# Kernel optimization log

Measured on AMD Instinct MI355X. Metric: run time of the kernel, lower is better.

## Reference

```python
import jax, jax.numpy as jnp
import numpy as np

N_NODES = 100000
N_EDGES = 1600000
IN_FEATS = 256
OUT_FEATS = 64


def setup_inputs() -> dict:
    key = jax.random.key(0)
    k1, k2, k3, k4, k5, k6 = jax.random.split(key, 6)
    x = jax.random.normal(k1, (N_NODES, IN_FEATS), dtype=jnp.float32)
    edge_src = jax.random.randint(k2, (N_EDGES,), 0, N_NODES, dtype=jnp.int32)
    edge_dst = jax.random.randint(k3, (N_EDGES,), 0, N_NODES, dtype=jnp.int32)
    edge_weight = jax.random.uniform(k4, (N_EDGES,), dtype=jnp.float32)
    # Linear(in_feats, out_feats) params (Kaiming-uniform-ish init scale)
    scale = 1.0 / np.sqrt(IN_FEATS)
    W = jax.random.uniform(k5, (IN_FEATS, OUT_FEATS), minval=-scale, maxval=scale, dtype=jnp.float32)
    b = jax.random.uniform(k6, (OUT_FEATS,), minval=-scale, maxval=scale, dtype=jnp.float32)
    return {"x": x, "edge_src": edge_src, "edge_dst": edge_dst,
            "edge_weight": edge_weight, "W": W, "b": b}


def reference(x, edge_src, edge_dst, edge_weight, W, b):
    # h = fc(x)
    h = x @ W + b                                   # [N, out_feats]
    # spmm(graph, h): out[dst] += w * h[src]  (weighted adjacency matvec)
    msgs = h[edge_src] * edge_weight[:, None]       # [E, out_feats]
    out = jax.ops.segment_sum(msgs, edge_dst, num_segments=N_NODES)
    return out
```

## Files before the change

### kernel.cpp

```cpp
#include <hip/hip_runtime.h>

#define IN_F 256
#define OUT_F 64
#define SORT_CHUNK 4096
#define BKT_SHIFT 7
#define BKT_NODES 128
#define MAX_NB 1024

typedef __attribute__((ext_vector_type(8))) short short8;
typedef __attribute__((ext_vector_type(4))) float f32x4;

static __device__ __forceinline__ short f2bf(float f) {
    union { float f; unsigned u; } v; v.f = f;
    unsigned r = v.u + 0x7FFFu + ((v.u >> 16) & 1u);
    return (short)(r >> 16);
}
static __device__ __forceinline__ float bf2f(short s) {
    return __int_as_float(((unsigned)(unsigned short)s) << 16);
}

__global__ __launch_bounds__(256)
void prep_w_kernel(const float* __restrict__ W, short* __restrict__ Wt) {
    int i = blockIdx.x * 256 + threadIdx.x;
    if (i < IN_F * OUT_F) {
        int k = i / OUT_F, n = i % OUT_F;
        Wt[n * IN_F + k] = f2bf(W[i]);
    }
}

__global__ __launch_bounds__(256, 4)
void fc_mfma_kernel(const float* __restrict__ x, const short* __restrict__ Wt,
                    const float* __restrict__ b, short* __restrict__ h, int nRows) {
    __shared__ short Wl[OUT_F * IN_F];
    {
        const uint4* src = (const uint4*)Wt;
        #pragma unroll
        for (int it = 0; it < 8; ++it) {
            int g = it * 256 + threadIdx.x;
            int n = g >> 5, s = g & 31;
            *(uint4*)((char*)Wl + n * 512 + (s ^ (n & 7)) * 16) = src[g];
        }
    }
    __syncthreads();

    const int wv = threadIdx.x >> 6;
    const int l  = threadIdx.x & 63;
    const int lr = l & 15;
    const int kg = l >> 4;

    const int rowbase = (blockIdx.x * 4 + wv) * 32;
    if (rowbase >= nRows) return;

    const int ar0 = min(rowbase + lr,      nRows - 1);
    const int ar1 = min(rowbase + 16 + lr, nRows - 1);
    const float* xp0 = x + (size_t)ar0 * IN_F + kg * 8;
    const float* xp1 = x + (size_t)ar1 * IN_F + kg * 8;

    f32x4 acc[2][4];
    #pragma unroll
    for (int m = 0; m < 2; ++m)
        #pragma unroll
        for (int n = 0; n < 4; ++n) acc[m][n] = (f32x4)0.f;

    #pragma unroll
    for (int kt = 0; kt < 8; ++kt) {
        const int K0 = kt * 32;
        float4 a0lo = *(const float4*)(xp0 + K0);
        float4 a0hi = *(const float4*)(xp0 + K0 + 4);
        float4 a1lo = *(const float4*)(xp1 + K0);
        float4 a1hi = *(const float4*)(xp1 + K0 + 4);

        short8 a0, a1;
        a0[0] = f2bf(a0lo.x); a0[1] = f2bf(a0lo.y);
        a0[2] = f2bf(a0lo.z); a0[3] = f2bf(a0lo.w);
        a0[4] = f2bf(a0hi.x); a0[5] = f2bf(a0hi.y);
        a0[6] = f2bf(a0hi.z); a0[7] = f2bf(a0hi.w);
        a1[0] = f2bf(a1lo.x); a1[1] = f2bf(a1lo.y);
        a1[2] = f2bf(a1lo.z); a1[3] = f2bf(a1lo.w);
        a1[4] = f2bf(a1hi.x); a1[5] = f2bf(a1hi.y);
        a1[6] = f2bf(a1hi.z); a1[7] = f2bf(a1hi.w);

        short8 bf[4];
        #pragma unroll
        for (int nt = 0; nt < 4; ++nt) {
            const int col = nt * 16 + lr;
            const int slot = (kt * 4 + kg) ^ (col & 7);
            bf[nt] = *(const short8*)((const char*)Wl + col * 512 + slot * 16);
        }
        #pragma unroll
        for (int nt = 0; nt < 4; ++nt) {
            acc[0][nt] = __builtin_amdgcn_mfma_f32_16x16x32_bf16(a0, bf[nt], acc[0][nt], 0, 0, 0);
            acc[1][nt] = __builtin_amdgcn_mfma_f32_16x16x32_bf16(a1, bf[nt], acc[1][nt], 0, 0, 0);
        }
    }

    #pragma unroll
    for (int m = 0; m < 2; ++m) {
        #pragma unroll
        for (int nt = 0; nt < 4; ++nt) {
            const int col = nt * 16 + lr;
            const float bias = b[col];
            #pragma unroll
            for (int j = 0; j < 4; ++j) {
                const int r = rowbase + m * 16 + kg * 4 + j;
                if (r < nRows)
                    h[(size_t)r * OUT_F + col] = f2bf(acc[m][nt][j] + bias);
            }
        }
    }
}

__global__ __launch_bounds__(256)
void bhist_kernel(const int* __restrict__ dst, int* __restrict__ counts,
                  int nE, int NB, int nSB) {
    __shared__ int lh[MAX_NB];
    for (int b = threadIdx.x; b < NB; b += 256) lh[b] = 0;
    __syncthreads();
    int base = blockIdx.x * SORT_CHUNK;
    int lim = min(nE, base + SORT_CHUNK);
    for (int e = base + threadIdx.x; e < lim; e += 256)
        atomicAdd(&lh[dst[e] >> BKT_SHIFT], 1);
    __syncthreads();
    for (int b = threadIdx.x; b < NB; b += 256)
        counts[b * nSB + blockIdx.x] = lh[b];
}

__global__ __launch_bounds__(256)
void scan1_kernel(const int* __restrict__ cnt, int* __restrict__ off,
                  int* __restrict__ part, int n) {
    __shared__ int sh[256];
    int base = blockIdx.x * 1024;
    int t = threadIdx.x;
    int v[4]; int s = 0;
    #pragma unroll
    for (int i = 0; i < 4; ++i) {
        int idx = base + t * 4 + i;
        v[i] = (idx < n) ? cnt[idx] : 0;
        s += v[i];
    }
    sh[t] = s;
    __syncthreads();
    for (int d = 1; d < 256; d <<= 1) {
        int val = (t >= d) ? sh[t - d] : 0;
        __syncthreads();
        sh[t] += val;
        __syncthreads();
    }
    if (t == 255) part[blockIdx.x] = sh[255];
    int run = (t == 0) ? 0 : sh[t - 1];
    #pragma unroll
    for (int i = 0; i < 4; ++i) {
        int idx = base + t * 4 + i;
        if (idx < n) off[idx] = run;
        run += v[i];
    }
}

__global__ __launch_bounds__(256)
void scan2_kernel(int* __restrict__ part, int nPart) {
    __shared__ int sh[256];
    int t = threadIdx.x;
    int v[4]; int s = 0;
    #pragma unroll
    for (int i = 0; i < 4; ++i) {
        int idx = t * 4 + i;
        v[i] = (idx < nPart) ? part[idx] : 0;
        s += v[i];
    }
    sh[t] = s;
    __syncthreads();
    for (int d = 1; d < 256; d <<= 1) {
        int val = (t >= d) ? sh[t - d] : 0;
        __syncthreads();
        sh[t] += val;
        __syncthreads();
    }
    int run = (t == 0) ? 0 : sh[t - 1];
    #pragma unroll
    for (int i = 0; i < 4; ++i) {
        int idx = t * 4 + i;
        if (idx < nPart) part[idx] = run;
        run += v[i];
    }
}

__global__ __launch_bounds__(256)
void scan3_kernel(int* __restrict__ off, const int* __restrict__ part, int n) {
    for (int i = blockIdx.x * blockDim.x + threadIdx.x; i < n;
         i += gridDim.x * blockDim.x)
        off[i] += part[i >> 10];
}

__global__ __launch_bounds__(256)
void bfill_kernel(const int* __restrict__ src, const int* __restrict__ dst,
                  const float* __restrict__ w, const int* __restrict__ bases,
                  int2* __restrict__ pack, int nE, int NB, int nSB) {
    __shared__ int cur[MAX_NB];
    for (int b = threadIdx.x; b < NB; b += 256)
        cur[b] = bases[b * nSB + blockIdx.x];
    __syncthreads();
    int base = blockIdx.x * SORT_CHUNK;
    int lim = min(nE, base + SORT_CHUNK);
    for (int e = base + threadIdx.x; e < lim; e += 256) {
        int d = dst[e];
        int p = atomicAdd(&cur[d >> BKT_SHIFT], 1);
        pack[p] = make_int2(src[e] | ((d & (BKT_NODES - 1)) << 17),
                            __float_as_int(w[e]));
    }
}

__global__ __launch_bounds__(256)
void nsort_kernel(const int2* __restrict__ pack, const int* __restrict__ bases,
                  int2* __restrict__ pack2, int* __restrict__ off,
                  int nRows, int nE, int NB, int nSB) {
    __shared__ int cnt[BKT_NODES];
    __shared__ int scn[BKT_NODES];
    const int b = blockIdx.x;
    const int tid = threadIdx.x;
    const int segStart = bases[b * nSB];
    const int segEnd = (b + 1 < NB) ? bases[(b + 1) * nSB] : nE;

    if (tid < BKT_NODES) cnt[tid] = 0;
    __syncthreads();
    for (int e = segStart + tid; e < segEnd; e += 256)
        atomicAdd(&cnt[(pack[e].x >> 17) & (BKT_NODES - 1)], 1);
    __syncthreads();

    if (tid < BKT_NODES) scn[tid] = cnt[tid];
    __syncthreads();
    for (int d = 1; d < BKT_NODES; d <<= 1) {
        int t = 0;
        if (tid < BKT_NODES && tid >= d) t = scn[tid - d];
        __syncthreads();
        if (tid < BKT_NODES) scn[tid] += t;
        __syncthreads();
    }

    const int node0 = b * BKT_NODES;
    const int ncnt = min(BKT_NODES, nRows - node0);
    if (tid < ncnt)
        off[node0 + tid] = segStart + scn[tid] - cnt[tid];
    if (tid == 0 && node0 + ncnt == nRows)
        off[nRows] = segEnd;
    __syncthreads();

    if (tid < BKT_NODES) cnt[tid] = segStart + scn[tid] - cnt[tid];
    __syncthreads();
    for (int e = segStart + tid; e < segEnd; e += 256) {
        int2 p = pack[e];
        int dl = (p.x >> 17) & (BKT_NODES - 1);
        int q = atomicAdd(&cnt[dl], 1);
        pack2[q] = make_int2(p.x & 0x1FFFF, p.y);
    }
}

__global__ __launch_bounds__(256)
void ngather_kernel(const short* __restrict__ h, const int* __restrict__ off,
                    const int2* __restrict__ pack2, float* __restrict__ out,
                    int nNodes) {
    int wid = (blockIdx.x * 256 + threadIdx.x) >> 6;
    int lane = threadIdx.x & 63;
    if (wid >= nNodes) return;
    int e = off[wid], end = off[wid + 1];
    const ushort* hu = (const ushort*)h;
    float acc = 0.f;
    for (; e + 8 <= end; e += 8) {
        int2 pk[8];
        #pragma unroll
        for (int i = 0; i < 8; ++i) pk[i] = pack2[e + i];
        float hv[8];
        #pragma unroll
        for (int i = 0; i < 8; ++i)
            hv[i] = bf2f((short)hu[(size_t)pk[i].x * OUT_F + lane]);
        #pragma unroll
        for (int i = 0; i < 8; ++i)
            acc = fmaf(__int_as_float(pk[i].y), hv[i], acc);
    }
    for (; e + 4 <= end; e += 4) {
        int2 pk[4];
        #pragma unroll
        for (int i = 0; i < 4; ++i) pk[i] = pack2[e + i];
        #pragma unroll
        for (int i = 0; i < 4; ++i)
            acc = fmaf(__int_as_float(pk[i].y),
                       bf2f((short)hu[(size_t)pk[i].x * OUT_F + lane]), acc);
    }
    for (; e < end; ++e) {
        int2 p = pack2[e];
        acc = fmaf(__int_as_float(p.y),
                   bf2f((short)hu[(size_t)p.x * OUT_F + lane]), acc);
    }
    out[(size_t)wid * OUT_F + lane] = acc;
}

__global__ __launch_bounds__(256)
void scatter_kernel(const short* __restrict__ h, const int* __restrict__ src,
                    const int* __restrict__ dst, const float* __restrict__ w,
                    float* __restrict__ out, int nE) {
    int t = blockIdx.x * 256 + threadIdx.x;
    int c = t & 15;
    int stride = (gridDim.x * 256) >> 4;
    for (int e = t >> 4; e < nE; e += stride) {
        int s = src[e];
        int d = dst[e];
        float ww = w[e];
        float* op = out + (size_t)d * OUT_F + c * 4;
        const short* hp = h + (size_t)s * OUT_F + c * 4;
        unsafeAtomicAdd(op + 0, ww * bf2f(hp[0]));
        unsafeAtomicAdd(op + 1, ww * bf2f(hp[1]));
        unsafeAtomicAdd(op + 2, ww * bf2f(hp[2]));
        unsafeAtomicAdd(op + 3, ww * bf2f(hp[3]));
    }
}

static inline size_t align256(size_t x) { return (x + 255) & ~(size_t)255; }

extern "C" void kernel_launch(void* const* d_in, const int* in_sizes, int n_in,
                              void* d_out, int out_size, void* d_ws, size_t ws_size,
                              hipStream_t stream) {
    const float* x    = (const float*)d_in[0];
    const int*   esrc = (const int*)d_in[1];
    const int*   edst = (const int*)d_in[2];
    const float* ew   = (const float*)d_in[3];
    const float* W    = (const float*)d_in[4];
    const float* b    = (const float*)d_in[5];

    int nRows = in_sizes[0] / IN_F;
    int nE    = in_sizes[1];

    int NB  = (nRows + BKT_NODES - 1) / BKT_NODES;
    int nSB = (nE + SORT_CHUNK - 1) / SORT_CHUNK;
    int nCnt = NB * nSB;
    int nPart = (nCnt + 1023) / 1024;

    char* p = (char*)d_ws;
    size_t hB    = align256((size_t)nRows * OUT_F * sizeof(short));
    size_t wtB   = align256((size_t)IN_F * OUT_F * sizeof(short));
    size_t cntB  = align256((size_t)nCnt * sizeof(int));
    size_t basB  = align256((size_t)nCnt * sizeof(int));
    size_t partB = align256((size_t)nPart * sizeof(int));
    size_t packB = align256((size_t)nE * sizeof(int2));
    size_t offB  = align256((size_t)(nRows + 1) * sizeof(int));
    size_t need  = hB + wtB + cntB + basB + partB + 2 * packB + offB;

    short* h      = (short*)p;  p += hB;
    short* Wt     = (short*)p;  p += wtB;
    int*   counts = (int*)p;    p += cntB;
    int*   bases  = (int*)p;    p += basB;
    int*   part   = (int*)p;    p += partB;
    int2*  pack   = (int2*)p;   p += packB;
    int2*  pack2  = (int2*)p;   p += packB;
    int*   off    = (int*)p;

    float* out = (float*)d_out;

    prep_w_kernel<<<(IN_F * OUT_F + 255) / 256, 256, 0, stream>>>(W, Wt);
    int fcBlocks = (nRows + 127) / 128;
    fc_mfma_kernel<<<fcBlocks, 256, 0, stream>>>(x, Wt, b, h, nRows);

    bool ok = (ws_size >= need) && (NB <= MAX_NB) && (nPart <= 1024) &&
              (nRows < (1 << 17));
    if (ok) {
        bhist_kernel<<<nSB, 256, 0, stream>>>(edst, counts, nE, NB, nSB);
        scan1_kernel<<<nPart, 256, 0, stream>>>(counts, bases, part, nCnt);
        scan2_kernel<<<1, 256, 0, stream>>>(part, nPart);
        scan3_kernel<<<512, 256, 0, stream>>>(bases, part, nCnt);
        bfill_kernel<<<nSB, 256, 0, stream>>>(esrc, edst, ew, bases, pack,
                                              nE, NB, nSB);
        nsort_kernel<<<NB, 256, 0, stream>>>(pack, bases, pack2, off,
                                             nRows, nE, NB, nSB);
        int gBlocks = (nRows * 64 + 255) / 256;
        ngather_kernel<<<gBlocks, 256, 0, stream>>>(h, off, pack2, out, nRows);
    } else {
        hipMemsetAsync(out, 0, (size_t)out_size * sizeof(float), stream);
        scatter_kernel<<<4096, 256, 0, stream>>>(h, esrc, edst, ew, out, nE);
    }
}
```

Measured before the change: 307.2 us.

## Fuse histogram into FC kernel, fold scan3 into consumers, vectorize sort loops

The bucket histogram now runs as extra blocks of the FC MFMA kernel, so the two independent stages overlap in one launch. The scan3 pass is removed: bfill and nsort add the partial block offset themselves when reading bases. The histogram, bfill and nsort loops are vectorized or unrolled by four to put more loads in flight. This removes two launches and one pass over the offset array, at the cost of more complex kernels. Mixing the two block types in one grid may also change how the FC blocks are scheduled.

```diff
diff --git a/kernel.cpp b/kernel.cpp
--- a/kernel.cpp
+++ b/kernel.cpp
@@ -29,9 +29,35 @@
 }
 
 __global__ __launch_bounds__(256, 4)
-void fc_mfma_kernel(const float* __restrict__ x, const short* __restrict__ Wt,
-                    const float* __restrict__ b, short* __restrict__ h, int nRows) {
-    __shared__ short Wl[OUT_F * IN_F];
+void fc_bhist_kernel(const float* __restrict__ x, const short* __restrict__ Wt,
+                     const float* __restrict__ bias, short* __restrict__ h,
+                     const int* __restrict__ dst, int* __restrict__ counts,
+                     int nRows, int nE, int NB, int nSB, int nHist) {
+    __shared__ __align__(16) char smem[OUT_F * IN_F * sizeof(short)];
+    if ((int)blockIdx.x < nHist) {
+        int* lh = (int*)smem;
+        const int cb = blockIdx.x;
+        for (int b0 = threadIdx.x; b0 < NB; b0 += 256) lh[b0] = 0;
+        __syncthreads();
+        const int base = cb * SORT_CHUNK;
+        const int lim = min(nE, base + SORT_CHUNK);
+        const int4* d4 = (const int4*)(dst + base);
+        const int n4 = (lim - base) >> 2;
+        for (int i = threadIdx.x; i < n4; i += 256) {
+            int4 v = d4[i];
+            atomicAdd(&lh[v.x >> BKT_SHIFT], 1);
+            atomicAdd(&lh[v.y >> BKT_SHIFT], 1);
+            atomicAdd(&lh[v.z >> BKT_SHIFT], 1);
+            atomicAdd(&lh[v.w >> BKT_SHIFT], 1);
+        }
+        for (int e = base + (n4 << 2) + threadIdx.x; e < lim; e += 256)
+            atomicAdd(&lh[dst[e] >> BKT_SHIFT], 1);
+        __syncthreads();
+        for (int b0 = threadIdx.x; b0 < NB; b0 += 256)
+            counts[b0 * nSB + cb] = lh[b0];
+        return;
+    }
+    short* Wl = (short*)smem;
     {
         const uint4* src = (const uint4*)Wt;
         #pragma unroll
@@ -48,7 +74,8 @@
     const int lr = l & 15;
     const int kg = l >> 4;
 
-    const int rowbase = (blockIdx.x * 4 + wv) * 32;
+    const int fb = blockIdx.x - nHist;
+    const int rowbase = (fb * 4 + wv) * 32;
     if (rowbase >= nRows) return;
 
     const int ar0 = min(rowbase + lr,      nRows - 1);
@@ -99,30 +126,15 @@
         #pragma unroll
         for (int nt = 0; nt < 4; ++nt) {
             const int col = nt * 16 + lr;
-            const float bias = b[col];
+            const float bb = bias[col];
             #pragma unroll
             for (int j = 0; j < 4; ++j) {
                 const int r = rowbase + m * 16 + kg * 4 + j;
                 if (r < nRows)
-                    h[(size_t)r * OUT_F + col] = f2bf(acc[m][nt][j] + bias);
+                    h[(size_t)r * OUT_F + col] = f2bf(acc[m][nt][j] + bb);
             }
         }
     }
-}
-
-__global__ __launch_bounds__(256)
-void bhist_kernel(const int* __restrict__ dst, int* __restrict__ counts,
-                  int nE, int NB, int nSB) {
-    __shared__ int lh[MAX_NB];
-    for (int b = threadIdx.x; b < NB; b += 256) lh[b] = 0;
-    __syncthreads();
-    int base = blockIdx.x * SORT_CHUNK;
-    int lim = min(nE, base + SORT_CHUNK);
-    for (int e = base + threadIdx.x; e < lim; e += 256)
-        atomicAdd(&lh[dst[e] >> BKT_SHIFT], 1);
-    __syncthreads();
-    for (int b = threadIdx.x; b < NB; b += 256)
-        counts[b * nSB + blockIdx.x] = lh[b];
 }
 
 __global__ __launch_bounds__(256)
@@ -185,23 +197,35 @@
 }
 
 __global__ __launch_bounds__(256)
-void scan3_kernel(int* __restrict__ off, const int* __restrict__ part, int n) {
-    for (int i = blockIdx.x * blockDim.x + threadIdx.x; i < n;
-         i += gridDim.x * blockDim.x)
-        off[i] += part[i >> 10];
-}
-
-__global__ __launch_bounds__(256)
 void bfill_kernel(const int* __restrict__ src, const int* __restrict__ dst,
                   const float* __restrict__ w, const int* __restrict__ bases,
-                  int2* __restrict__ pack, int nE, int NB, int nSB) {
+                  const int* __restrict__ part, int2* __restrict__ pack,
+                  int nE, int NB, int nSB) {
     __shared__ int cur[MAX_NB];
-    for (int b = threadIdx.x; b < NB; b += 256)
-        cur[b] = bases[b * nSB + blockIdx.x];
-    __syncthreads();
-    int base = blockIdx.x * SORT_CHUNK;
-    int lim = min(nE, base + SORT_CHUNK);
-    for (int e = base + threadIdx.x; e < lim; e += 256) {
+    const int cb = blockIdx.x;
+    for (int b0 = threadIdx.x; b0 < NB; b0 += 256) {
+        int idx = b0 * nSB + cb;
+        cur[b0] = bases[idx] + part[idx >> 10];
+    }
+    __syncthreads();
+    const int base = cb * SORT_CHUNK;
+    const int lim = min(nE, base + SORT_CHUNK);
+    const int4* s4 = (const int4*)(src + base);
+    const int4* d4 = (const int4*)(dst + base);
+    const float4* w4 = (const float4*)(w + base);
+    const int n4 = (lim - base) >> 2;
+    for (int i = threadIdx.x; i < n4; i += 256) {
+        int4 s = s4[i]; int4 d = d4[i]; float4 ww = w4[i];
+        int p0 = atomicAdd(&cur[d.x >> BKT_SHIFT], 1);
+        pack[p0] = make_int2(s.x | ((d.x & (BKT_NODES - 1)) << 17), __float_as_int(ww.x));
+        int p1 = atomicAdd(&cur[d.y >> BKT_SHIFT], 1);
+        pack[p1] = make_int2(s.y | ((d.y & (BKT_NODES - 1)) << 17), __float_as_int(ww.y));
+        int p2 = atomicAdd(&cur[d.z >> BKT_SHIFT], 1);
+        pack[p2] = make_int2(s.z | ((d.z & (BKT_NODES - 1)) << 17), __float_as_int(ww.z));
+        int p3 = atomicAdd(&cur[d.w >> BKT_SHIFT], 1);
+        pack[p3] = make_int2(s.w | ((d.w & (BKT_NODES - 1)) << 17), __float_as_int(ww.w));
+    }
+    for (int e = base + (n4 << 2) + threadIdx.x; e < lim; e += 256) {
         int d = dst[e];
         int p = atomicAdd(&cur[d >> BKT_SHIFT], 1);
         pack[p] = make_int2(src[e] | ((d & (BKT_NODES - 1)) << 17),
@@ -211,19 +235,35 @@
 
 __global__ __launch_bounds__(256)
 void nsort_kernel(const int2* __restrict__ pack, const int* __restrict__ bases,
-                  int2* __restrict__ pack2, int* __restrict__ off,
-                  int nRows, int nE, int NB, int nSB) {
+                  const int* __restrict__ part, int2* __restrict__ pack2,
+                  int* __restrict__ off, int nRows, int nE, int NB, int nSB) {
     __shared__ int cnt[BKT_NODES];
     __shared__ int scn[BKT_NODES];
     const int b = blockIdx.x;
     const int tid = threadIdx.x;
-    const int segStart = bases[b * nSB];
-    const int segEnd = (b + 1 < NB) ? bases[(b + 1) * nSB] : nE;
+    const int i0 = b * nSB;
+    const int segStart = bases[i0] + part[i0 >> 10];
+    int segEnd = nE;
+    if (b + 1 < NB) {
+        int i1 = (b + 1) * nSB;
+        segEnd = bases[i1] + part[i1 >> 10];
+    }
 
     if (tid < BKT_NODES) cnt[tid] = 0;
     __syncthreads();
-    for (int e = segStart + tid; e < segEnd; e += 256)
-        atomicAdd(&cnt[(pack[e].x >> 17) & (BKT_NODES - 1)], 1);
+    {
+        int e = segStart + tid;
+        for (; e + 768 < segEnd; e += 1024) {
+            int a0 = pack[e].x, a1 = pack[e + 256].x;
+            int a2 = pack[e + 512].x, a3 = pack[e + 768].x;
+            atomicAdd(&cnt[(a0 >> 17) & (BKT_NODES - 1)], 1);
+            atomicAdd(&cnt[(a1 >> 17) & (BKT_NODES - 1)], 1);
+            atomicAdd(&cnt[(a2 >> 17) & (BKT_NODES - 1)], 1);
+            atomicAdd(&cnt[(a3 >> 17) & (BKT_NODES - 1)], 1);
+        }
+        for (; e < segEnd; e += 256)
+            atomicAdd(&cnt[(pack[e].x >> 17) & (BKT_NODES - 1)], 1);
+    }
     __syncthreads();
 
     if (tid < BKT_NODES) scn[tid] = cnt[tid];
@@ -246,11 +286,25 @@
 
     if (tid < BKT_NODES) cnt[tid] = segStart + scn[tid] - cnt[tid];
     __syncthreads();
-    for (int e = segStart + tid; e < segEnd; e += 256) {
-        int2 p = pack[e];
-        int dl = (p.x >> 17) & (BKT_NODES - 1);
-        int q = atomicAdd(&cnt[dl], 1);
-        pack2[q] = make_int2(p.x & 0x1FFFF, p.y);
+    {
+        int e = segStart + tid;
+        for (; e + 768 < segEnd; e += 1024) {
+            int2 p0 = pack[e], p1 = pack[e + 256];
+            int2 p2 = pack[e + 512], p3 = pack[e + 768];
+            int q0 = atomicAdd(&cnt[(p0.x >> 17) & (BKT_NODES - 1)], 1);
+            pack2[q0] = make_int2(p0.x & 0x1FFFF, p0.y);
+            int q1 = atomicAdd(&cnt[(p1.x >> 17) & (BKT_NODES - 1)], 1);
+            pack2[q1] = make_int2(p1.x & 0x1FFFF, p1.y);
+            int q2 = atomicAdd(&cnt[(p2.x >> 17) & (BKT_NODES - 1)], 1);
+            pack2[q2] = make_int2(p2.x & 0x1FFFF, p2.y);
+            int q3 = atomicAdd(&cnt[(p3.x >> 17) & (BKT_NODES - 1)], 1);
+            pack2[q3] = make_int2(p3.x & 0x1FFFF, p3.y);
+        }
+        for (; e < segEnd; e += 256) {
+            int2 p = pack[e];
+            int q = atomicAdd(&cnt[(p.x >> 17) & (BKT_NODES - 1)], 1);
+            pack2[q] = make_int2(p.x & 0x1FFFF, p.y);
+        }
     }
 }
 
@@ -354,20 +408,21 @@
 
     float* out = (float*)d_out;
 
-    prep_w_kernel<<<(IN_F * OUT_F + 255) / 256, 256, 0, stream>>>(W, Wt);
-    int fcBlocks = (nRows + 127) / 128;
-    fc_mfma_kernel<<<fcBlocks, 256, 0, stream>>>(x, Wt, b, h, nRows);
-
     bool ok = (ws_size >= need) && (NB <= MAX_NB) && (nPart <= 1024) &&
               (nRows < (1 << 17));
+    int nHist = ok ? nSB : 0;
+    int fcBlocks = (nRows + 127) / 128;
+
+    prep_w_kernel<<<(IN_F * OUT_F + 255) / 256, 256, 0, stream>>>(W, Wt);
+    fc_bhist_kernel<<<nHist + fcBlocks, 256, 0, stream>>>(
+        x, Wt, b, h, edst, counts, nRows, nE, NB, nSB, nHist);
+
     if (ok) {
-        bhist_kernel<<<nSB, 256, 0, stream>>>(edst, counts, nE, NB, nSB);
         scan1_kernel<<<nPart, 256, 0, stream>>>(counts, bases, part, nCnt);
         scan2_kernel<<<1, 256, 0, stream>>>(part, nPart);
-        scan3_kernel<<<512, 256, 0, stream>>>(bases, part, nCnt);
-        bfill_kernel<<<nSB, 256, 0, stream>>>(esrc, edst, ew, bases, pack,
-                                              nE, NB, nSB);
-        nsort_kernel<<<NB, 256, 0, stream>>>(pack, bases, pack2, off,
+        bfill_kernel<<<nSB, 256, 0, stream>>>(esrc, edst, ew, bases, part,
+                                              pack, nE, NB, nSB);
+        nsort_kernel<<<NB, 256, 0, stream>>>(pack, bases, part, pack2, off,
                                              nRows, nE, NB, nSB);
         int gBlocks = (nRows * 64 + 255) / 256;
         ngather_kernel<<<gBlocks, 256, 0, stream>>>(h, off, pack2, out, nRows);
```

After: 286.4 us. -6.7%, faster.
